# Performance work log

Hardware: AMD Instinct MI355X
Metric: run time of the kernel (lower is better)

The kernel has to match this reference:

```python
import jax, jax.numpy as jnp
import numpy as np

DIM = 1024
HEADS = 16


def setup_inputs() -> dict:
    key = jax.random.key(0)
    ks = jax.random.split(key, 5)
    x = jax.random.normal(ks[0], (2, 2048, DIM), dtype=jnp.float32)
    # nn.Linear init-like scaling
    qkv_w = jax.random.normal(ks[1], (3 * DIM, DIM), dtype=jnp.float32) * (1.0 / np.sqrt(DIM))
    qkv_b = jax.random.normal(ks[2], (3 * DIM,), dtype=jnp.float32) * 0.02
    proj_w = jax.random.normal(ks[3], (DIM, DIM), dtype=jnp.float32) * (1.0 / np.sqrt(DIM))
    proj_b = jax.random.normal(ks[4], (DIM,), dtype=jnp.float32) * 0.02
    return {"x": x, "qkv_w": qkv_w, "qkv_b": qkv_b, "proj_w": proj_w, "proj_b": proj_b}


def reference(x, qkv_w, qkv_b, proj_w, proj_b):
    B, N, C = x.shape
    H = HEADS
    Dh = C // H
    scale = Dh ** -0.5
    # qkv: [B, N, 3C] -> [3, B, H, N, Dh]
    qkv = (x @ qkv_w.T + qkv_b).reshape(B, N, 3, H, Dh).transpose(2, 0, 3, 1, 4)
    q, k, v = qkv[0], qkv[1], qkv[2]
    attn = jnp.einsum('bhnd,bhmd->bhnm', q, k) * scale
    attn = jax.nn.softmax(attn, axis=-1)
    out = jnp.einsum('bhnm,bhmd->bhnd', attn, v)  # [B, H, N, Dh]
    out = out.transpose(0, 2, 1, 3).reshape(B, N, C)
    return out @ proj_w.T + proj_b
```

## Files before the change

### kernel.cpp

```cpp
#include <hip/hip_runtime.h>
#include <stdint.h>

#define DIM    1024
#define NHEADS 16
#define DH     64
#define SEQ    2048
#define BATCH  2
#define BHEADS (BATCH * NHEADS)
#define MROWS  (BATCH * SEQ)
#define SL2E   0.18033688011112042f

typedef __attribute__((ext_vector_type(8))) short bf16x8;
typedef __attribute__((ext_vector_type(4))) float f32x4;
typedef unsigned short ushort_t;

#define GLDS(gp, lp) __builtin_amdgcn_global_load_lds( \
    (__attribute__((address_space(1))) void*)(gp), \
    (__attribute__((address_space(3))) void*)(lp), 16, 0, 0)

__device__ inline ushort_t f2bf(float f) {
    unsigned u = __builtin_bit_cast(unsigned, f);
    u += 0x7FFFu + ((u >> 16) & 1u);
    return (ushort_t)(u >> 16);
}

__global__ __launch_bounds__(256) void cvt_kernel(
    const float* __restrict__ s0, const float* __restrict__ s1, const float* __restrict__ s2,
    ushort_t* __restrict__ d0, ushort_t* __restrict__ d1, ushort_t* __restrict__ d2)
{
    const int N0 = MROWS * DIM;
    const int N1 = 3 * DIM * DIM;
    const int N2 = DIM * DIM;
    int e = (blockIdx.x * 256 + threadIdx.x) << 2;
    const float* src; ushort_t* dst;
    if (e < N0)                { src = s0 + e;             dst = d0 + e; }
    else if (e < N0 + N1)      { src = s1 + (e - N0);      dst = d1 + (e - N0); }
    else if (e < N0 + N1 + N2) { src = s2 + (e - N0 - N1); dst = d2 + (e - N0 - N1); }
    else return;
    float4 f = *(const float4*)src;
    ushort4 o;
    o.x = f2bf(f.x); o.y = f2bf(f.y); o.z = f2bf(f.z); o.w = f2bf(f.w);
    *(ushort4*)dst = o;
}

__global__ __launch_bounds__(256) void qkv_gemm(
    const ushort_t* __restrict__ A, const ushort_t* __restrict__ W,
    const float* __restrict__ bias,
    ushort_t* __restrict__ Qw, ushort_t* __restrict__ Kw, ushort_t* __restrict__ Vt)
{
    __shared__ union {
        ushort_t stage[2][2][128 * 64];
        ushort_t T[128 * 136];
    } sm;

    const int tid  = threadIdx.x;
    const int lane = tid & 63;
    const int wave = tid >> 6;
    const int quad = lane >> 4;
    const int l16  = lane & 15;
    const int wm   = (wave >> 1) * 64;
    const int wn   = (wave & 1) * 64;
    const int bm   = blockIdx.x * 128;
    const int bn   = blockIdx.y * 128;
    const int Rl   = lane >> 3;
    const int pp   = lane & 7;

    f32x4 acc[4][4];
    for (int i = 0; i < 4; i++)
        for (int j = 0; j < 4; j++)
            for (int r = 0; r < 4; r++) acc[i][j][r] = 0.f;

    for (int j = 0; j < 4; j++) {
        int Rb = j * 32 + wave * 8;
        int R  = Rb + Rl;
        int c  = pp ^ (R & 7);
        GLDS(A + (size_t)(bm + R) * DIM + c * 8, sm.stage[0][0] + Rb * 64 + lane * 8);
        GLDS(W + (size_t)(bn + R) * DIM + c * 8, sm.stage[0][1] + Rb * 64 + lane * 8);
    }

    const int NT = DIM / 64;
    for (int t = 0; t < NT; t++) {
        if (t < NT - 1) {
            int kk = (t + 1) * 64;
            ushort_t* As1 = sm.stage[(t + 1) & 1][0];
            ushort_t* Bs1 = sm.stage[(t + 1) & 1][1];
            for (int j = 0; j < 4; j++) {
                int Rb = j * 32 + wave * 8;
                int R  = Rb + Rl;
                int c  = pp ^ (R & 7);
                GLDS(A + (size_t)(bm + R) * DIM + kk + c * 8, As1 + Rb * 64 + lane * 8);
                GLDS(W + (size_t)(bn + R) * DIM + kk + c * 8, Bs1 + Rb * 64 + lane * 8);
            }
            __asm volatile("s_waitcnt vmcnt(8)" ::: "memory");
        } else {
            __asm volatile("s_waitcnt vmcnt(0)" ::: "memory");
        }
        __asm volatile("s_barrier" ::: "memory");

        const ushort_t* Asb = sm.stage[t & 1][0];
        const ushort_t* Bsb = sm.stage[t & 1][1];
        for (int kh = 0; kh < 2; kh++) {
            bf16x8 a[4], b[4];
            for (int mi = 0; mi < 4; mi++) {
                int r = wm + mi * 16 + l16;
                a[mi] = *(const bf16x8*)(Asb + r * 64 + (((kh * 4 + quad) ^ (r & 7)) << 3));
            }
            for (int ni = 0; ni < 4; ni++) {
                int r = wn + ni * 16 + l16;
                b[ni] = *(const bf16x8*)(Bsb + r * 64 + (((kh * 4 + quad) ^ (r & 7)) << 3));
            }
            for (int mi = 0; mi < 4; mi++)
                for (int ni = 0; ni < 4; ni++)
                    acc[mi][ni] = __builtin_amdgcn_mfma_f32_16x16x32_bf16(a[mi], b[ni], acc[mi][ni], 0, 0, 0);
        }
        __asm volatile("s_waitcnt lgkmcnt(0)" ::: "memory");
        __asm volatile("s_barrier" ::: "memory");
    }

    const int three = bn >> 10;
    const float scale = (three == 0) ? SL2E : 1.0f;
    for (int ni = 0; ni < 4; ni++) {
        int cl   = wn + ni * 16 + l16;
        float bv = bias[bn + cl];
        for (int mi = 0; mi < 4; mi++)
            for (int reg = 0; reg < 4; reg++) {
                int r = wm + mi * 16 + quad * 4 + reg;
                sm.T[r * 136 + cl] = f2bf((acc[mi][ni][reg] + bv) * scale);
            }
    }
    __syncthreads();

    const int b = bm >> 11, npos0 = bm & 2047;
    if (three < 2) {
        int r = tid >> 1, hh = tid & 1;
        int hc = (bn + hh * 64) & 1023;
        int h  = hc >> 6;
        ushort_t* dst = (three == 0 ? Qw : Kw) + ((size_t)(b * NHEADS + h) * SEQ + npos0 + r) * DH;
        const ushort_t* srcp = sm.T + r * 136 + hh * 64;
        for (int s = 0; s < 8; s++)
            *(uint4*)(dst + s * 8) = *(const uint4*)(srcp + s * 8);
    } else {
        int c = tid & 127, hh = tid >> 7;
        int hc = (bn + c) & 1023;
        int h  = hc >> 6, d = hc & 63;
        ushort_t* dst = Vt + ((size_t)(b * NHEADS + h) * DH + d) * SEQ + npos0 + hh * 64;
        for (int s = 0; s < 8; s++) {
            union { ushort_t u[8]; uint4 v; } tmp;
            for (int k2 = 0; k2 < 8; k2++)
                tmp.u[k2] = sm.T[(hh * 64 + s * 8 + k2) * 136 + c];
            *(uint4*)(dst + s * 8) = tmp.v;
        }
    }
}

struct AttnSmem {
    ushort_t KV[2][2][2][32 * 64];
    ushort_t QP[128 * 64];
};
union AttnSmemU {
    AttnSmem m;
    float Lb[128][66];
};

__global__ __launch_bounds__(512, 4) void attn_kernel(
    const ushort_t* __restrict__ Qw, const ushort_t* __restrict__ Kw,
    const ushort_t* __restrict__ Vt, ushort_t* __restrict__ Ao)
{
    __shared__ AttnSmemU sh;

    const int tid  = threadIdx.x;
    const int lane = tid & 63;
    const int wave = tid >> 6;
    const int grp  = wave >> 2;
    const int wg   = wave & 3;
    const int quad = lane >> 4;
    const int l16  = lane & 15;
    const int bh   = blockIdx.y;
    const int q0   = blockIdx.x * 128;
    const int Rl   = lane >> 3;
    const int pp   = lane & 7;

    const ushort_t* Qh = Qw + (size_t)bh * SEQ * DH;
    const ushort_t* Kh = Kw + (size_t)bh * SEQ * DH;
    const ushort_t* Vh = Vt + (size_t)bh * DH * SEQ;

    for (int j = 0; j < 2; j++) {
        int Rb = j * 64 + wave * 8;
        int R  = Rb + Rl;
        int c  = pp ^ (R & 7);
        GLDS(Qh + (size_t)(q0 + R) * DH + c * 8, sh.m.QP + Rb * 64 + lane * 8);
    }
    {
        int t  = grp;
        int Rk = wg * 8 + Rl;
        int ck = pp ^ (Rk & 7);
        GLDS(Kh + (size_t)(t * 32 + Rk) * DH + ck * 8, sh.m.KV[0][grp][0] + wg * 512 + lane * 8);
        int Rv = wg * 16 + (lane >> 2);
        int pv = lane & 3;
        int cv = pv ^ ((Rv >> 1) & 3);
        GLDS(Vh + (size_t)Rv * SEQ + t * 32 + cv * 8, sh.m.KV[0][grp][1] + wg * 512 + lane * 8);
    }
    __syncthreads();

    bf16x8 qf[2][2];
    for (int mi = 0; mi < 2; mi++)
        for (int kh = 0; kh < 2; kh++) {
            int r = wg * 32 + mi * 16 + l16;
            qf[mi][kh] = *(const bf16x8*)(sh.m.QP + r * 64 + (((kh * 4 + quad) ^ (r & 7)) << 3));
        }
    __syncthreads();

    bf16x8 vones;
    for (int i = 0; i < 8; i++) vones[i] = (short)0x3F80;

    f32x4 oacc[2][4], liacc[2];
    for (int mi = 0; mi < 2; mi++) {
        for (int r = 0; r < 4; r++) liacc[mi][r] = 0.f;
        for (int d = 0; d < 4; d++)
            for (int r = 0; r < 4; r++) oacc[mi][d][r] = 0.f;
    }

    ushort_t* Pw = sh.m.QP + wave * 1024;

    const int NIT = 32;
    for (int it = 0; it < NIT; it++) {
        const int phase = it & 1;
        if (it < NIT - 1) {
            int np = phase ^ 1;
            int t  = 2 * (it + 1) + grp;
            int Rk = wg * 8 + Rl;
            int ck = pp ^ (Rk & 7);
            GLDS(Kh + (size_t)(t * 32 + Rk) * DH + ck * 8, sh.m.KV[np][grp][0] + wg * 512 + lane * 8);
            int Rv = wg * 16 + (lane >> 2);
            int pv = lane & 3;
            int cv = pv ^ ((Rv >> 1) & 3);
            GLDS(Vh + (size_t)Rv * SEQ + t * 32 + cv * 8, sh.m.KV[np][grp][1] + wg * 512 + lane * 8);
        }
        const ushort_t* Ksb = sh.m.KV[phase][grp][0];
        const ushort_t* Vsb = sh.m.KV[phase][grp][1];

        f32x4 s[2][2];
        for (int mi = 0; mi < 2; mi++)
            for (int nf = 0; nf < 2; nf++)
                for (int r = 0; r < 4; r++) s[mi][nf][r] = 0.f;
        for (int kh = 0; kh < 2; kh++)
            for (int nf = 0; nf < 2; nf++) {
                int r = nf * 16 + l16;
                bf16x8 kf = *(const bf16x8*)(Ksb + r * 64 + (((kh * 4 + quad) ^ (r & 7)) << 3));
                s[0][nf] = __builtin_amdgcn_mfma_f32_16x16x32_bf16(kf, qf[0][kh], s[0][nf], 0, 0, 0);
                s[1][nf] = __builtin_amdgcn_mfma_f32_16x16x32_bf16(kf, qf[1][kh], s[1][nf], 0, 0, 0);
            }

        for (int mi = 0; mi < 2; mi++) {
            int row = mi * 16 + l16;
            int swz = (row >> 1) & 3;
            for (int nf = 0; nf < 2; nf++) {
                unsigned u0 = __builtin_bit_cast(unsigned, __builtin_amdgcn_exp2f(s[mi][nf][0])) + 0x8000u;
                unsigned u1 = __builtin_bit_cast(unsigned, __builtin_amdgcn_exp2f(s[mi][nf][1])) + 0x8000u;
                unsigned u2 = __builtin_bit_cast(unsigned, __builtin_amdgcn_exp2f(s[mi][nf][2])) + 0x8000u;
                unsigned u3 = __builtin_bit_cast(unsigned, __builtin_amdgcn_exp2f(s[mi][nf][3])) + 0x8000u;
                uint2 pk;
                pk.x = __builtin_amdgcn_perm(u1, u0, 0x07060302u);
                pk.y = __builtin_amdgcn_perm(u3, u2, 0x07060302u);
                int jp = (nf * 2 + (quad >> 1)) ^ swz;
                *(uint2*)(Pw + row * 32 + jp * 8 + (quad & 1) * 4) = pk;
            }
        }

        bf16x8 pf[2];
        for (int mi = 0; mi < 2; mi++) {
            int row = mi * 16 + l16;
            int jp  = quad ^ ((row >> 1) & 3);
            pf[mi] = *(const bf16x8*)(Pw + row * 32 + jp * 8);
        }

        liacc[0] = __builtin_amdgcn_mfma_f32_16x16x32_bf16(pf[0], vones, liacc[0], 0, 0, 0);
        liacc[1] = __builtin_amdgcn_mfma_f32_16x16x32_bf16(pf[1], vones, liacc[1], 0, 0, 0);

        for (int df = 0; df < 4; df++) {
            int r  = df * 16 + l16;
            int jp = quad ^ ((r >> 1) & 3);
            bf16x8 vf = *(const bf16x8*)(Vsb + r * 32 + jp * 8);
            oacc[0][df] = __builtin_amdgcn_mfma_f32_16x16x32_bf16(pf[0], vf, oacc[0][df], 0, 0, 0);
            oacc[1][df] = __builtin_amdgcn_mfma_f32_16x16x32_bf16(pf[1], vf, oacc[1][df], 0, 0, 0);
        }

        __syncthreads();
    }

    const int b = bh >> 4, h = bh & 15;
    if (grp == 1) {
        for (int mi = 0; mi < 2; mi++)
            for (int reg = 0; reg < 4; reg++) {
                int row = wg * 32 + mi * 16 + quad * 4 + reg;
                for (int df = 0; df < 4; df++)
                    sh.Lb[row][df * 16 + l16] = oacc[mi][df][reg];
                if (l16 == 0) sh.Lb[row][64] = liacc[mi][reg];
            }
    }
    __syncthreads();
    if (grp == 0) {
        for (int mi = 0; mi < 2; mi++)
            for (int reg = 0; reg < 4; reg++) {
                int row   = wg * 32 + mi * 16 + quad * 4 + reg;
                float inv = 1.0f / (liacc[mi][reg] + sh.Lb[row][64]);
                int grow  = q0 + row;
                for (int df = 0; df < 4; df++) {
                    int col = df * 16 + l16;
                    float o = oacc[mi][df][reg] + sh.Lb[row][col];
                    Ao[((size_t)b * SEQ + grow) * DIM + h * 64 + col] = f2bf(o * inv);
                }
            }
    }
}

__global__ __launch_bounds__(256, 4) void proj_gemm(
    const ushort_t* __restrict__ A, const ushort_t* __restrict__ W,
    const float* __restrict__ bias, float* __restrict__ Cout)
{
    __shared__ ushort_t Asd[2][128 * 64];
    __shared__ ushort_t Bsd[2][64 * 64];

    const int tid  = threadIdx.x;
    const int lane = tid & 63;
    const int wave = tid >> 6;
    const int quad = lane >> 4;
    const int l16  = lane & 15;
    const int wm   = (wave >> 1) * 64;
    const int wn   = (wave & 1) * 32;
    const int bm   = blockIdx.x * 128;
    const int bn   = blockIdx.y * 64;
    const int Rl   = lane >> 3;
    const int pp   = lane & 7;

    f32x4 acc[4][2];
    for (int i = 0; i < 4; i++)
        for (int j = 0; j < 2; j++)
            for (int r = 0; r < 4; r++) acc[i][j][r] = 0.f;

    for (int j = 0; j < 4; j++) {
        int Rb = j * 32 + wave * 8;
        int R  = Rb + Rl;
        int c  = pp ^ (R & 7);
        GLDS(A + (size_t)(bm + R) * DIM + c * 8, Asd[0] + Rb * 64 + lane * 8);
    }
    for (int j = 0; j < 2; j++) {
        int Rb = j * 32 + wave * 8;
        int R  = Rb + Rl;
        int c  = pp ^ (R & 7);
        GLDS(W + (size_t)(bn + R) * DIM + c * 8, Bsd[0] + Rb * 64 + lane * 8);
    }

    const int NT = DIM / 64;
    for (int t = 0; t < NT; t++) {
        if (t < NT - 1) {
            int kk = (t + 1) * 64;
            ushort_t* As1 = Asd[(t + 1) & 1];
            ushort_t* Bs1 = Bsd[(t + 1) & 1];
            for (int j = 0; j < 4; j++) {
                int Rb = j * 32 + wave * 8;
                int R  = Rb + Rl;
                int c  = pp ^ (R & 7);
                GLDS(A + (size_t)(bm + R) * DIM + kk + c * 8, As1 + Rb * 64 + lane * 8);
            }
            for (int j = 0; j < 2; j++) {
                int Rb = j * 32 + wave * 8;
                int R  = Rb + Rl;
                int c  = pp ^ (R & 7);
                GLDS(W + (size_t)(bn + R) * DIM + kk + c * 8, Bs1 + Rb * 64 + lane * 8);
            }
            __asm volatile("s_waitcnt vmcnt(6)" ::: "memory");
        } else {
            __asm volatile("s_waitcnt vmcnt(0)" ::: "memory");
        }
        __asm volatile("s_barrier" ::: "memory");

        const ushort_t* Asb = Asd[t & 1];
        const ushort_t* Bsb = Bsd[t & 1];
        for (int kh = 0; kh < 2; kh++) {
            bf16x8 a[4], b[2];
            for (int mi = 0; mi < 4; mi++) {
                int r = wm + mi * 16 + l16;
                a[mi] = *(const bf16x8*)(Asb + r * 64 + (((kh * 4 + quad) ^ (r & 7)) << 3));
            }
            for (int ni = 0; ni < 2; ni++) {
                int r = wn + ni * 16 + l16;
                b[ni] = *(const bf16x8*)(Bsb + r * 64 + (((kh * 4 + quad) ^ (r & 7)) << 3));
            }
            for (int mi = 0; mi < 4; mi++)
                for (int ni = 0; ni < 2; ni++)
                    acc[mi][ni] = __builtin_amdgcn_mfma_f32_16x16x32_bf16(a[mi], b[ni], acc[mi][ni], 0, 0, 0);
        }
        __asm volatile("s_waitcnt lgkmcnt(0)" ::: "memory");
        __asm volatile("s_barrier" ::: "memory");
    }

    for (int mi = 0; mi < 4; mi++) {
        for (int ni = 0; ni < 2; ni++) {
            int col  = bn + wn + ni * 16 + l16;
            float bv = bias[col];
            for (int reg = 0; reg < 4; reg++) {
                int row = bm + wm + mi * 16 + quad * 4 + reg;
                Cout[(size_t)row * DIM + col] = acc[mi][ni][reg] + bv;
            }
        }
    }
}

extern "C" void kernel_launch(void* const* d_in, const int* in_sizes, int n_in,
                              void* d_out, int out_size, void* d_ws, size_t ws_size,
                              hipStream_t stream) {
    const float* x      = (const float*)d_in[0];
    const float* qkv_w  = (const float*)d_in[1];
    const float* qkv_b  = (const float*)d_in[2];
    const float* proj_w = (const float*)d_in[3];
    const float* proj_b = (const float*)d_in[4];
    float* out = (float*)d_out;

    ushort_t* xb      = (ushort_t*)d_ws;
    ushort_t* qkv_wb  = xb      + (size_t)MROWS * DIM;
    ushort_t* proj_wb = qkv_wb  + (size_t)3 * DIM * DIM;
    ushort_t* Qw      = proj_wb + (size_t)DIM * DIM;
    ushort_t* Kw      = Qw      + (size_t)BHEADS * SEQ * DH;
    ushort_t* Vt      = Kw      + (size_t)BHEADS * SEQ * DH;
    ushort_t* Ao      = Vt      + (size_t)BHEADS * SEQ * DH;

    const int total_cvt = MROWS * DIM + 3 * DIM * DIM + DIM * DIM;
    cvt_kernel<<<total_cvt / (4 * 256), 256, 0, stream>>>(x, qkv_w, proj_w, xb, qkv_wb, proj_wb);
    qkv_gemm<<<dim3(MROWS / 128, (3 * DIM) / 128), 256, 0, stream>>>(xb, qkv_wb, qkv_b, Qw, Kw, Vt);
    attn_kernel<<<dim3(SEQ / 128, BHEADS), 512, 0, stream>>>(Qw, Kw, Vt, Ao);
    proj_gemm<<<dim3(MROWS / 128, DIM / 64), 256, 0, stream>>>(Ao, proj_wb, proj_b, out);
}
```

Measured before the change: 182.5 us.

## Triple-buffer K/V tiles and feed P to MFMA from registers

Extends the attention K/V shared-memory ring from two to three stages. Prefetch now runs two tiles ahead, and the per-iteration __syncthreads is replaced by a hand-written s_waitcnt vmcnt(2) plus s_barrier, so one load group can stay in flight. The exponentiated probabilities are packed straight into registers and fed to 16x16x16 bf16 MFMAs, which removes the LDS round trip for P. Costs are more LDS per block (a possible occupancy drop), twice as many smaller MFMA instructions, and fragile inline-asm wait counts.

Result: no change. 181.5 us (-0.6%).

```diff
diff --git a/kernel.cpp b/kernel.cpp
--- a/kernel.cpp
+++ b/kernel.cpp
@@ -11,12 +11,24 @@
 #define SL2E   0.18033688011112042f
 
 typedef __attribute__((ext_vector_type(8))) short bf16x8;
+typedef __attribute__((ext_vector_type(4))) short bf16x4;
 typedef __attribute__((ext_vector_type(4))) float f32x4;
 typedef unsigned short ushort_t;
 
 #define GLDS(gp, lp) __builtin_amdgcn_global_load_lds( \
     (__attribute__((address_space(1))) void*)(gp), \
     (__attribute__((address_space(3))) void*)(lp), 16, 0, 0)
+
+#if __has_builtin(__builtin_amdgcn_mfma_f32_16x16x16bf16_1k)
+#define MFMA16(a, b, c) __builtin_amdgcn_mfma_f32_16x16x16bf16_1k(a, b, c, 0, 0, 0)
+#else
+static __device__ inline f32x4 mfma16_asm(bf16x4 a, bf16x4 b, f32x4 c) {
+    asm volatile("s_nop 1\n\tv_mfma_f32_16x16x16_bf16 %0, %1, %2, %0"
+                 : "+v"(c) : "v"(a), "v"(b));
+    return c;
+}
+#define MFMA16(a, b, c) mfma16_asm(a, b, c)
+#endif
 
 __device__ inline ushort_t f2bf(float f) {
     unsigned u = __builtin_bit_cast(unsigned, f);
@@ -154,7 +166,7 @@
 }
 
 struct AttnSmem {
-    ushort_t KV[2][2][2][32 * 64];
+    ushort_t KV[3][2][2][32 * 64];
     ushort_t QP[128 * 64];
 };
 union AttnSmemU {
@@ -190,15 +202,15 @@
         int c  = pp ^ (R & 7);
         GLDS(Qh + (size_t)(q0 + R) * DH + c * 8, sh.m.QP + Rb * 64 + lane * 8);
     }
-    {
-        int t  = grp;
+    for (int t = 0; t < 2; t++) {
+        int tile = 2 * t + grp;
         int Rk = wg * 8 + Rl;
         int ck = pp ^ (Rk & 7);
-        GLDS(Kh + (size_t)(t * 32 + Rk) * DH + ck * 8, sh.m.KV[0][grp][0] + wg * 512 + lane * 8);
+        GLDS(Kh + (size_t)(tile * 32 + Rk) * DH + ck * 8, sh.m.KV[t][grp][0] + wg * 512 + lane * 8);
         int Rv = wg * 16 + (lane >> 2);
         int pv = lane & 3;
         int cv = pv ^ ((Rv >> 1) & 3);
-        GLDS(Vh + (size_t)Rv * SEQ + t * 32 + cv * 8, sh.m.KV[0][grp][1] + wg * 512 + lane * 8);
+        GLDS(Vh + (size_t)Rv * SEQ + tile * 32 + cv * 8, sh.m.KV[t][grp][1] + wg * 512 + lane * 8);
     }
     __syncthreads();
 
@@ -208,10 +220,9 @@
             int r = wg * 32 + mi * 16 + l16;
             qf[mi][kh] = *(const bf16x8*)(sh.m.QP + r * 64 + (((kh * 4 + quad) ^ (r & 7)) << 3));
         }
-    __syncthreads();
-
-    bf16x8 vones;
-    for (int i = 0; i < 8; i++) vones[i] = (short)0x3F80;
+
+    bf16x4 vones4;
+    for (int i = 0; i < 4; i++) vones4[i] = (short)0x3F80;
 
     f32x4 oacc[2][4], liacc[2];
     for (int mi = 0; mi < 2; mi++) {
@@ -220,73 +231,74 @@
             for (int r = 0; r < 4; r++) oacc[mi][d][r] = 0.f;
     }
 
-    ushort_t* Pw = sh.m.QP + wave * 1024;
+    const int swzv = (l16 >> 1) & 3;
 
     const int NIT = 32;
+    int cur = 0;
     for (int it = 0; it < NIT; it++) {
-        const int phase = it & 1;
-        if (it < NIT - 1) {
-            int np = phase ^ 1;
-            int t  = 2 * (it + 1) + grp;
+        if (it < NIT - 2) {
+            int pidx = cur + 2; if (pidx >= 3) pidx -= 3;
+            int tile = 2 * (it + 2) + grp;
             int Rk = wg * 8 + Rl;
             int ck = pp ^ (Rk & 7);
-            GLDS(Kh + (size_t)(t * 32 + Rk) * DH + ck * 8, sh.m.KV[np][grp][0] + wg * 512 + lane * 8);
+            GLDS(Kh + (size_t)(tile * 32 + Rk) * DH + ck * 8, sh.m.KV[pidx][grp][0] + wg * 512 + lane * 8);
             int Rv = wg * 16 + (lane >> 2);
             int pv = lane & 3;
             int cv = pv ^ ((Rv >> 1) & 3);
-            GLDS(Vh + (size_t)Rv * SEQ + t * 32 + cv * 8, sh.m.KV[np][grp][1] + wg * 512 + lane * 8);
-        }
-        const ushort_t* Ksb = sh.m.KV[phase][grp][0];
-        const ushort_t* Vsb = sh.m.KV[phase][grp][1];
-
-        f32x4 s[2][2];
+            GLDS(Vh + (size_t)Rv * SEQ + tile * 32 + cv * 8, sh.m.KV[pidx][grp][1] + wg * 512 + lane * 8);
+        }
+        const ushort_t* Ksb = sh.m.KV[cur][grp][0];
+        const ushort_t* Vsb = sh.m.KV[cur][grp][1];
+
+        f32x4 s2[2][2];
         for (int mi = 0; mi < 2; mi++)
             for (int nf = 0; nf < 2; nf++)
-                for (int r = 0; r < 4; r++) s[mi][nf][r] = 0.f;
+                for (int r = 0; r < 4; r++) s2[mi][nf][r] = 0.f;
         for (int kh = 0; kh < 2; kh++)
             for (int nf = 0; nf < 2; nf++) {
                 int r = nf * 16 + l16;
                 bf16x8 kf = *(const bf16x8*)(Ksb + r * 64 + (((kh * 4 + quad) ^ (r & 7)) << 3));
-                s[0][nf] = __builtin_amdgcn_mfma_f32_16x16x32_bf16(kf, qf[0][kh], s[0][nf], 0, 0, 0);
-                s[1][nf] = __builtin_amdgcn_mfma_f32_16x16x32_bf16(kf, qf[1][kh], s[1][nf], 0, 0, 0);
-            }
-
-        for (int mi = 0; mi < 2; mi++) {
-            int row = mi * 16 + l16;
-            int swz = (row >> 1) & 3;
+                s2[0][nf] = __builtin_amdgcn_mfma_f32_16x16x32_bf16(kf, qf[0][kh], s2[0][nf], 0, 0, 0);
+                s2[1][nf] = __builtin_amdgcn_mfma_f32_16x16x32_bf16(kf, qf[1][kh], s2[1][nf], 0, 0, 0);
+            }
+
+        bf16x4 pa[2][2];
+        for (int mi = 0; mi < 2; mi++)
             for (int nf = 0; nf < 2; nf++) {
-                unsigned u0 = __builtin_bit_cast(unsigned, __builtin_amdgcn_exp2f(s[mi][nf][0])) + 0x8000u;
-                unsigned u1 = __builtin_bit_cast(unsigned, __builtin_amdgcn_exp2f(s[mi][nf][1])) + 0x8000u;
-                unsigned u2 = __builtin_bit_cast(unsigned, __builtin_amdgcn_exp2f(s[mi][nf][2])) + 0x8000u;
-                unsigned u3 = __builtin_bit_cast(unsigned, __builtin_amdgcn_exp2f(s[mi][nf][3])) + 0x8000u;
+                unsigned u0 = __builtin_bit_cast(unsigned, __builtin_amdgcn_exp2f(s2[mi][nf][0])) + 0x8000u;
+                unsigned u1 = __builtin_bit_cast(unsigned, __builtin_amdgcn_exp2f(s2[mi][nf][1])) + 0x8000u;
+                unsigned u2 = __builtin_bit_cast(unsigned, __builtin_amdgcn_exp2f(s2[mi][nf][2])) + 0x8000u;
+                unsigned u3 = __builtin_bit_cast(unsigned, __builtin_amdgcn_exp2f(s2[mi][nf][3])) + 0x8000u;
                 uint2 pk;
                 pk.x = __builtin_amdgcn_perm(u1, u0, 0x07060302u);
                 pk.y = __builtin_amdgcn_perm(u3, u2, 0x07060302u);
-                int jp = (nf * 2 + (quad >> 1)) ^ swz;
-                *(uint2*)(Pw + row * 32 + jp * 8 + (quad & 1) * 4) = pk;
-            }
-        }
-
-        bf16x8 pf[2];
-        for (int mi = 0; mi < 2; mi++) {
-            int row = mi * 16 + l16;
-            int jp  = quad ^ ((row >> 1) & 3);
-            pf[mi] = *(const bf16x8*)(Pw + row * 32 + jp * 8);
-        }
-
-        liacc[0] = __builtin_amdgcn_mfma_f32_16x16x32_bf16(pf[0], vones, liacc[0], 0, 0, 0);
-        liacc[1] = __builtin_amdgcn_mfma_f32_16x16x32_bf16(pf[1], vones, liacc[1], 0, 0, 0);
-
-        for (int df = 0; df < 4; df++) {
-            int r  = df * 16 + l16;
-            int jp = quad ^ ((r >> 1) & 3);
-            bf16x8 vf = *(const bf16x8*)(Vsb + r * 32 + jp * 8);
-            oacc[0][df] = __builtin_amdgcn_mfma_f32_16x16x32_bf16(pf[0], vf, oacc[0][df], 0, 0, 0);
-            oacc[1][df] = __builtin_amdgcn_mfma_f32_16x16x32_bf16(pf[1], vf, oacc[1][df], 0, 0, 0);
-        }
-
-        __syncthreads();
-    }
+                pa[mi][nf] = __builtin_bit_cast(bf16x4, pk);
+            }
+
+        for (int nf = 0; nf < 2; nf++) {
+            liacc[0] = MFMA16(pa[0][nf], vones4, liacc[0]);
+            liacc[1] = MFMA16(pa[1][nf], vones4, liacc[1]);
+            for (int df = 0; df < 4; df++) {
+                int row = df * 16 + l16;
+                int jp  = (2 * nf + (quad >> 1)) ^ swzv;
+                bf16x4 vf = *(const bf16x4*)(Vsb + row * 32 + jp * 8 + (quad & 1) * 4);
+                oacc[0][df] = MFMA16(pa[0][nf], vf, oacc[0][df]);
+                oacc[1][df] = MFMA16(pa[1][nf], vf, oacc[1][df]);
+            }
+        }
+
+        if (it < NIT - 2) {
+            __asm volatile("s_waitcnt vmcnt(2) lgkmcnt(0)" ::: "memory");
+            __asm volatile("s_barrier" ::: "memory");
+        } else if (it == NIT - 2) {
+            __asm volatile("s_waitcnt vmcnt(0) lgkmcnt(0)" ::: "memory");
+            __asm volatile("s_barrier" ::: "memory");
+        }
+        cur++; if (cur == 3) cur = 0;
+    }
+
+    __asm volatile("s_nop 7\n\ts_nop 7");
+    __syncthreads();
 
     const int b = bh >> 4, h = bh & 15;
     if (grp == 1) {
```

## Rework attention inner loop around 32x32x16 MFMA with register-resident P

Applied to the files above, without the earlier changes.

Rewrites the attention kernel to use 32x32x16 bf16 MFMAs. The S-tile output layout is fed directly as the A operand of the PV product, so the P round-trip through shared memory and the ones-vector MFMA for row sums are gone; row sums are now accumulated in registers. To make the P-from-S reuse line up, the V transpose in the QKV kernel permutes key positions within each block, and the shared-memory layout is split into Q, K and V regions. Synchronisation moves to explicit waitcnt/barrier asm with a single barrier pair per iteration. This adds register pressure from the f32x16 accumulators and depends on the key-permutation being exactly consistent between kernels.

New measurement: 184.0 us. Within noise of the previous version (+0.8%).

```diff
diff --git a/kernel.cpp b/kernel.cpp
--- a/kernel.cpp
+++ b/kernel.cpp
@@ -12,6 +12,7 @@
 
 typedef __attribute__((ext_vector_type(8))) short bf16x8;
 typedef __attribute__((ext_vector_type(4))) float f32x4;
+typedef __attribute__((ext_vector_type(16))) float f32x16;
 typedef unsigned short ushort_t;
 
 #define GLDS(gp, lp) __builtin_amdgcn_global_load_lds( \
@@ -146,16 +147,20 @@
         ushort_t* dst = Vt + ((size_t)(b * NHEADS + h) * DH + d) * SEQ + npos0 + hh * 64;
         for (int s = 0; s < 8; s++) {
             union { ushort_t u[8]; uint4 v; } tmp;
-            for (int k2 = 0; k2 < 8; k2++)
-                tmp.u[k2] = sm.T[(hh * 64 + s * 8 + k2) * 136 + c];
+            for (int k2 = 0; k2 < 8; k2++) {
+                int o  = hh * 64 + s * 8 + k2;
+                int po = (o & ~12) | ((o & 4) << 1) | ((o & 8) >> 1);
+                tmp.u[k2] = sm.T[po * 136 + c];
+            }
             *(uint4*)(dst + s * 8) = tmp.v;
         }
     }
 }
 
 struct AttnSmem {
-    ushort_t KV[2][2][2][32 * 64];
-    ushort_t QP[128 * 64];
+    ushort_t Qs[128 * 64];
+    ushort_t Ks[2][2][32 * 64];
+    ushort_t Vs[2][64 * 64];
 };
 union AttnSmemU {
     AttnSmem m;
@@ -173,8 +178,8 @@
     const int wave = tid >> 6;
     const int grp  = wave >> 2;
     const int wg   = wave & 3;
-    const int quad = lane >> 4;
-    const int l16  = lane & 15;
+    const int hi   = lane >> 5;
+    const int l32  = lane & 31;
     const int bh   = blockIdx.y;
     const int q0   = blockIdx.x * 128;
     const int Rl   = lane >> 3;
@@ -188,129 +193,125 @@
         int Rb = j * 64 + wave * 8;
         int R  = Rb + Rl;
         int c  = pp ^ (R & 7);
-        GLDS(Qh + (size_t)(q0 + R) * DH + c * 8, sh.m.QP + Rb * 64 + lane * 8);
+        GLDS(Qh + (size_t)(q0 + R) * DH + c * 8, sh.m.Qs + Rb * 64 + lane * 8);
     }
     {
-        int t  = grp;
-        int Rk = wg * 8 + Rl;
-        int ck = pp ^ (Rk & 7);
-        GLDS(Kh + (size_t)(t * 32 + Rk) * DH + ck * 8, sh.m.KV[0][grp][0] + wg * 512 + lane * 8);
-        int Rv = wg * 16 + (lane >> 2);
-        int pv = lane & 3;
-        int cv = pv ^ ((Rv >> 1) & 3);
-        GLDS(Vh + (size_t)Rv * SEQ + t * 32 + cv * 8, sh.m.KV[0][grp][1] + wg * 512 + lane * 8);
-    }
-    __syncthreads();
-
-    bf16x8 qf[2][2];
-    for (int mi = 0; mi < 2; mi++)
-        for (int kh = 0; kh < 2; kh++) {
-            int r = wg * 32 + mi * 16 + l16;
-            qf[mi][kh] = *(const bf16x8*)(sh.m.QP + r * 64 + (((kh * 4 + quad) ^ (r & 7)) << 3));
-        }
-    __syncthreads();
-
-    bf16x8 vones;
-    for (int i = 0; i < 8; i++) vones[i] = (short)0x3F80;
-
-    f32x4 oacc[2][4], liacc[2];
-    for (int mi = 0; mi < 2; mi++) {
-        for (int r = 0; r < 4; r++) liacc[mi][r] = 0.f;
-        for (int d = 0; d < 4; d++)
-            for (int r = 0; r < 4; r++) oacc[mi][d][r] = 0.f;
-    }
-
-    ushort_t* Pw = sh.m.QP + wave * 1024;
+        int R = wg * 8 + Rl;
+        int c = pp ^ (R & 7);
+        GLDS(Kh + (size_t)(grp * 32 + R) * DH + c * 8, sh.m.Ks[0][grp] + wg * 512 + lane * 8);
+        int Rd = wave * 8 + Rl;
+        int cv = pp ^ (Rd & 7);
+        GLDS(Vh + (size_t)Rd * SEQ + cv * 8, sh.m.Vs[0] + wave * 512 + lane * 8);
+    }
+
+    f32x16 oacc[2];
+#pragma unroll
+    for (int dh = 0; dh < 2; dh++)
+#pragma unroll
+        for (int i = 0; i < 16; i++) oacc[dh][i] = 0.f;
+    float liacc = 0.f;
+    bf16x8 qf[4];
 
     const int NIT = 32;
     for (int it = 0; it < NIT; it++) {
-        const int phase = it & 1;
         if (it < NIT - 1) {
-            int np = phase ^ 1;
-            int t  = 2 * (it + 1) + grp;
-            int Rk = wg * 8 + Rl;
-            int ck = pp ^ (Rk & 7);
-            GLDS(Kh + (size_t)(t * 32 + Rk) * DH + ck * 8, sh.m.KV[np][grp][0] + wg * 512 + lane * 8);
-            int Rv = wg * 16 + (lane >> 2);
-            int pv = lane & 3;
-            int cv = pv ^ ((Rv >> 1) & 3);
-            GLDS(Vh + (size_t)Rv * SEQ + t * 32 + cv * 8, sh.m.KV[np][grp][1] + wg * 512 + lane * 8);
-        }
-        const ushort_t* Ksb = sh.m.KV[phase][grp][0];
-        const ushort_t* Vsb = sh.m.KV[phase][grp][1];
-
-        f32x4 s[2][2];
-        for (int mi = 0; mi < 2; mi++)
-            for (int nf = 0; nf < 2; nf++)
-                for (int r = 0; r < 4; r++) s[mi][nf][r] = 0.f;
-        for (int kh = 0; kh < 2; kh++)
-            for (int nf = 0; nf < 2; nf++) {
-                int r = nf * 16 + l16;
-                bf16x8 kf = *(const bf16x8*)(Ksb + r * 64 + (((kh * 4 + quad) ^ (r & 7)) << 3));
-                s[0][nf] = __builtin_amdgcn_mfma_f32_16x16x32_bf16(kf, qf[0][kh], s[0][nf], 0, 0, 0);
-                s[1][nf] = __builtin_amdgcn_mfma_f32_16x16x32_bf16(kf, qf[1][kh], s[1][nf], 0, 0, 0);
-            }
-
-        for (int mi = 0; mi < 2; mi++) {
-            int row = mi * 16 + l16;
-            int swz = (row >> 1) & 3;
-            for (int nf = 0; nf < 2; nf++) {
-                unsigned u0 = __builtin_bit_cast(unsigned, __builtin_amdgcn_exp2f(s[mi][nf][0])) + 0x8000u;
-                unsigned u1 = __builtin_bit_cast(unsigned, __builtin_amdgcn_exp2f(s[mi][nf][1])) + 0x8000u;
-                unsigned u2 = __builtin_bit_cast(unsigned, __builtin_amdgcn_exp2f(s[mi][nf][2])) + 0x8000u;
-                unsigned u3 = __builtin_bit_cast(unsigned, __builtin_amdgcn_exp2f(s[mi][nf][3])) + 0x8000u;
-                uint2 pk;
-                pk.x = __builtin_amdgcn_perm(u1, u0, 0x07060302u);
-                pk.y = __builtin_amdgcn_perm(u3, u2, 0x07060302u);
-                int jp = (nf * 2 + (quad >> 1)) ^ swz;
-                *(uint2*)(Pw + row * 32 + jp * 8 + (quad & 1) * 4) = pk;
-            }
-        }
-
-        bf16x8 pf[2];
-        for (int mi = 0; mi < 2; mi++) {
-            int row = mi * 16 + l16;
-            int jp  = quad ^ ((row >> 1) & 3);
-            pf[mi] = *(const bf16x8*)(Pw + row * 32 + jp * 8);
-        }
-
-        liacc[0] = __builtin_amdgcn_mfma_f32_16x16x32_bf16(pf[0], vones, liacc[0], 0, 0, 0);
-        liacc[1] = __builtin_amdgcn_mfma_f32_16x16x32_bf16(pf[1], vones, liacc[1], 0, 0, 0);
-
-        for (int df = 0; df < 4; df++) {
-            int r  = df * 16 + l16;
-            int jp = quad ^ ((r >> 1) & 3);
-            bf16x8 vf = *(const bf16x8*)(Vsb + r * 32 + jp * 8);
-            oacc[0][df] = __builtin_amdgcn_mfma_f32_16x16x32_bf16(pf[0], vf, oacc[0][df], 0, 0, 0);
-            oacc[1][df] = __builtin_amdgcn_mfma_f32_16x16x32_bf16(pf[1], vf, oacc[1][df], 0, 0, 0);
-        }
-
-        __syncthreads();
-    }
+            int nb = (it + 1) & 1;
+            int kb = (it + 1) * 64;
+            int R  = wg * 8 + Rl;
+            int c  = pp ^ (R & 7);
+            GLDS(Kh + (size_t)(kb + grp * 32 + R) * DH + c * 8, sh.m.Ks[nb][grp] + wg * 512 + lane * 8);
+            int Rd = wave * 8 + Rl;
+            int cv = pp ^ (Rd & 7);
+            GLDS(Vh + (size_t)Rd * SEQ + kb + cv * 8, sh.m.Vs[nb] + wave * 512 + lane * 8);
+            __asm volatile("s_waitcnt vmcnt(2)" ::: "memory");
+        } else {
+            __asm volatile("s_waitcnt vmcnt(0)" ::: "memory");
+        }
+        __asm volatile("s_barrier" ::: "memory");
+
+        if (it == 0) {
+            int qr = wg * 32 + l32;
+#pragma unroll
+            for (int kt = 0; kt < 4; kt++)
+                qf[kt] = *(const bf16x8*)(sh.m.Qs + qr * 64 + (((2 * kt + hi) ^ (qr & 7)) << 3));
+        }
+
+        const ushort_t* Ksb = sh.m.Ks[it & 1][grp];
+        const ushort_t* Vsb = sh.m.Vs[it & 1];
+
+        f32x16 S;
+#pragma unroll
+        for (int i = 0; i < 16; i++) S[i] = 0.f;
+#pragma unroll
+        for (int kt = 0; kt < 4; kt++) {
+            bf16x8 kf = *(const bf16x8*)(Ksb + l32 * 64 + (((2 * kt + hi) ^ (l32 & 7)) << 3));
+            S = __builtin_amdgcn_mfma_f32_32x32x16_bf16(kf, qf[kt], S, 0, 0, 0);
+        }
+
+        unsigned Dw[8];
+        float lis = 0.f;
+#pragma unroll
+        for (int m = 0; m < 8; m++) {
+            float p0 = __builtin_amdgcn_exp2f(S[2 * m]);
+            float p1 = __builtin_amdgcn_exp2f(S[2 * m + 1]);
+            lis += p0 + p1;
+            unsigned u0 = __builtin_bit_cast(unsigned, p0) + 0x8000u;
+            unsigned u1 = __builtin_bit_cast(unsigned, p1) + 0x8000u;
+            Dw[m] = __builtin_amdgcn_perm(u1, u0, 0x07060302u);
+        }
+        liacc += lis;
+        union { unsigned u[4]; bf16x8 v; } pc0, pc1;
+        pc0.u[0] = Dw[0]; pc0.u[1] = Dw[1]; pc0.u[2] = Dw[2]; pc0.u[3] = Dw[3];
+        pc1.u[0] = Dw[4]; pc1.u[1] = Dw[5]; pc1.u[2] = Dw[6]; pc1.u[3] = Dw[7];
+        bf16x8 pa[2] = { pc0.v, pc1.v };
+
+#pragma unroll
+        for (int kt = 0; kt < 2; kt++)
+#pragma unroll
+            for (int dh = 0; dh < 2; dh++) {
+                int dr = dh * 32 + l32;
+                bf16x8 vf = *(const bf16x8*)(Vsb + dr * 64 + (((grp * 4 + 2 * kt + hi) ^ (dr & 7)) << 3));
+                oacc[dh] = __builtin_amdgcn_mfma_f32_32x32x16_bf16(pa[kt], vf, oacc[dh], 0, 0, 0);
+            }
+
+        if (it < NIT - 1) {
+            __asm volatile("s_waitcnt lgkmcnt(0)" ::: "memory");
+            __asm volatile("s_barrier" ::: "memory");
+        }
+    }
+
+    float li2 = liacc + __shfl_xor(liacc, 32, 64);
+
+    __asm volatile("s_waitcnt lgkmcnt(0)" ::: "memory");
+    __syncthreads();
 
     const int b = bh >> 4, h = bh & 15;
     if (grp == 1) {
-        for (int mi = 0; mi < 2; mi++)
-            for (int reg = 0; reg < 4; reg++) {
-                int row = wg * 32 + mi * 16 + quad * 4 + reg;
-                for (int df = 0; df < 4; df++)
-                    sh.Lb[row][df * 16 + l16] = oacc[mi][df][reg];
-                if (l16 == 0) sh.Lb[row][64] = liacc[mi][reg];
-            }
+#pragma unroll
+        for (int dh = 0; dh < 2; dh++)
+#pragma unroll
+            for (int reg = 0; reg < 16; reg++) {
+                int row = wg * 32 + (reg & 3) + 8 * (reg >> 2) + 4 * hi;
+                sh.Lb[row][dh * 32 + l32] = oacc[dh][reg];
+            }
+        if (lane < 32) sh.Lb[wg * 32 + lane][64] = li2;
+    } else {
+        if (lane < 32) sh.Lb[wg * 32 + lane][65] = li2;
     }
     __syncthreads();
     if (grp == 0) {
-        for (int mi = 0; mi < 2; mi++)
-            for (int reg = 0; reg < 4; reg++) {
-                int row   = wg * 32 + mi * 16 + quad * 4 + reg;
-                float inv = 1.0f / (liacc[mi][reg] + sh.Lb[row][64]);
-                int grow  = q0 + row;
-                for (int df = 0; df < 4; df++) {
-                    int col = df * 16 + l16;
-                    float o = oacc[mi][df][reg] + sh.Lb[row][col];
-                    Ao[((size_t)b * SEQ + grow) * DIM + h * 64 + col] = f2bf(o * inv);
-                }
-            }
+#pragma unroll
+        for (int reg = 0; reg < 16; reg++) {
+            int row = wg * 32 + (reg & 3) + 8 * (reg >> 2) + 4 * hi;
+            float2 lv = *(const float2*)&sh.Lb[row][64];
+            float inv = 1.0f / (lv.x + lv.y);
+            int grow = q0 + row;
+#pragma unroll
+            for (int dh = 0; dh < 2; dh++) {
+                float o = oacc[dh][reg] + sh.Lb[row][dh * 32 + l32];
+                Ao[((size_t)b * SEQ + grow) * DIM + h * 64 + dh * 32 + l32] = f2bf(o * inv);
+            }
+        }
     }
 }
 
```
